# Kernel tuning notes

Measured on AMD Instinct MI355X. Metric: run time of the kernel, lower is better.

The kernel has to match this reference:

```python
import jax, jax.numpy as jnp
import numpy as np

DIM = 192
HEADS = 6
WS = 7          # window size
SS = 3          # shift size
MLP_H = int(DIM * 4.0)
EPS_LN = 1e-5


def _static_tables():
    # Swin-v2 log-spaced continuous relative coords table: (1, 2*WS-1, 2*WS-1, 2)
    ch = np.arange(-(WS - 1), WS, dtype=np.float32)
    cw = np.arange(-(WS - 1), WS, dtype=np.float32)
    t = np.stack(np.meshgrid(ch, cw, indexing='ij'), axis=-1)[None]
    t[..., 0] /= (WS - 1)
    t[..., 1] /= (WS - 1)
    t *= 7.0
    t = np.sign(t) * np.log2(np.abs(t) + 1.0) / np.log2(7.0)
    # relative position index: (WS*WS, WS*WS)
    coords = np.stack(np.meshgrid(np.arange(WS), np.arange(WS), indexing='ij'))
    cf = coords.reshape(2, -1)
    rc = (cf[:, :, None] - cf[:, None, :]).transpose(1, 2, 0)
    rc[..., 0] += WS - 1
    rc[..., 1] += WS - 1
    rc[..., 0] *= 2 * WS - 1
    rpi = rc.sum(-1)
    return jnp.asarray(t, jnp.float32), jnp.asarray(rpi, jnp.int32)


def _attn_mask(H, W):
    # shifted-window mask: (nW, N, N) with 0 / -100
    img = np.zeros((H, W), np.float32)
    cnt = 0
    for hs in (slice(0, -WS), slice(-WS, -SS), slice(-SS, None)):
        for ws in (slice(0, -WS), slice(-WS, -SS), slice(-SS, None)):
            img[hs, ws] = cnt
            cnt += 1
    mw = img.reshape(H // WS, WS, W // WS, WS).transpose(0, 2, 1, 3).reshape(-1, WS * WS)
    am = mw[:, None, :] - mw[:, :, None]
    am = np.where(am != 0, -100.0, 0.0).astype(np.float32)
    return jnp.asarray(am)


def _ln(x, w, b):
    m = x.mean(-1, keepdims=True)
    v = ((x - m) ** 2).mean(-1, keepdims=True)
    return (x - m) / jnp.sqrt(v + EPS_LN) * w + b


def setup_inputs() -> dict:
    key = jax.random.key(0)
    ks = jax.random.split(key, 16)
    d = DIM
    inp = {
        'x': jax.random.normal(ks[0], (32, 56, 56, d), jnp.float32),
        'qkv_w': jax.random.normal(ks[1], (3 * d, d), jnp.float32) * (2.0 / d) ** 0.5,
        'qkv_b': jnp.full((3 * d,), 0.01, jnp.float32),
        'proj_w': jax.random.normal(ks[2], (d, d), jnp.float32) * (2.0 / d) ** 0.5,
        'proj_b': jnp.full((d,), 0.01, jnp.float32),
        'logit_scale': jnp.log(10.0 * jnp.ones((HEADS, 1, 1), jnp.float32)),
        'cpb_w1': jax.random.normal(ks[3], (512, 2), jnp.float32) * (2.0 / 2) ** 0.5,
        'cpb_b1': jnp.full((512,), 0.01, jnp.float32),
        'cpb_w2': jax.random.normal(ks[4], (HEADS, 512), jnp.float32) * (2.0 / 512) ** 0.5,
        'norm1_w': jnp.ones((d,), jnp.float32),
        'norm1_b': jnp.zeros((d,), jnp.float32),
        'norm2_w': jnp.ones((d,), jnp.float32),
        'norm2_b': jnp.zeros((d,), jnp.float32),
        'fc1_w': jax.random.normal(ks[5], (MLP_H, d), jnp.float32) * (2.0 / d) ** 0.5,
        'fc1_b': jnp.full((MLP_H,), 0.01, jnp.float32),
        'fc2_w': jax.random.normal(ks[6], (d, MLP_H), jnp.float32) * (2.0 / MLP_H) ** 0.5,
        'fc2_b': jnp.full((d,), 0.01, jnp.float32),
    }
    return inp


def reference(x, qkv_w, qkv_b, proj_w, proj_b, logit_scale, cpb_w1, cpb_b1, cpb_w2,
              norm1_w, norm1_b, norm2_w, norm2_b, fc1_w, fc1_b, fc2_w, fc2_b):
    B, H, W, C = x.shape
    N = WS * WS
    hd = C // HEADS
    table, rpi = _static_tables()
    mask = _attn_mask(H, W)  # (nW, N, N)
    nW = mask.shape[0]

    shortcut = x
    # cyclic shift + window partition: (B*nW, N, C)
    xs = jnp.roll(x, (-SS, -SS), axis=(1, 2))
    xw = xs.reshape(B, H // WS, WS, W // WS, WS, C).transpose(0, 1, 3, 2, 4, 5).reshape(-1, N, C)

    qkv = xw @ qkv_w.T + qkv_b
    qkv = qkv.reshape(-1, N, 3, HEADS, hd).transpose(2, 0, 3, 1, 4)
    q, k, v = qkv[0], qkv[1], qkv[2]  # (B_, H, N, hd)

    qn = q / jnp.clip(jnp.linalg.norm(q, axis=-1, keepdims=True), 1e-12)
    kn = k / jnp.clip(jnp.linalg.norm(k, axis=-1, keepdims=True), 1e-12)
    scale = jnp.exp(jnp.minimum(logit_scale, jnp.log(100.0)))  # (HEADS,1,1)
    attn = jnp.einsum('bhnd,bhmd->bhnm', qn, kn) * scale

    # CPB-MLP relative position bias
    hbt = jax.nn.leaky_relu(table @ cpb_w1.T + cpb_b1, 0.01) @ cpb_w2.T  # (1,13,13,HEADS)
    bias_table = hbt.reshape(-1, HEADS)
    rpb = bias_table[rpi.reshape(-1)].reshape(N, N, HEADS).transpose(2, 0, 1)
    attn = attn + (14.0 * jax.nn.sigmoid(rpb))[None]

    # shifted-window mask + softmax
    attn = attn.reshape(B, nW, HEADS, N, N) + mask[None, :, None]
    attn = jax.nn.softmax(attn.reshape(-1, HEADS, N, N), axis=-1)

    out = jnp.einsum('bhnm,bhmd->bnhd', attn, v).reshape(-1, N, C)
    out = out @ proj_w.T + proj_b

    # window reverse + reverse shift
    out = out.reshape(B, H // WS, W // WS, WS, WS, C).transpose(0, 1, 3, 2, 4, 5).reshape(B, H, W, C)
    out = jnp.roll(out, (SS, SS), axis=(1, 2))

    # post-norm residuals (Swin-v2 style)
    x1 = shortcut + _ln(out, norm1_w, norm1_b)
    mlp = jax.nn.gelu(x1 @ fc1_w.T + fc1_b, approximate=False) @ fc2_w.T + fc2_b
    return x1 + _ln(mlp, norm2_w, norm2_b)
```

## Files before the change

### kernel.cpp

```cpp
#include <hip/hip_runtime.h>
#include <math.h>

#define CDIM 192
#define NHEADS 6
#define HDIM 32
#define WSZ 7
#define NTOK 49
#define SHIFT 3
#define HW 56
#define MLPH 768
#define NTOKENS 100352
#define QKS 576
#define XS 200
#define VTS 72
#define PPS 72
#define LS 196
#define QPS 72
#define AS2 200
#define HS2 200
#define OS2 196

typedef __attribute__((ext_vector_type(8))) short short8;
typedef __attribute__((ext_vector_type(4))) float floatx4;
typedef unsigned short ushort_t;
typedef unsigned int uint_t;

__device__ __forceinline__ ushort_t f2b(float f) {
  uint_t u = __float_as_uint(f);
  u = (u + 0x7FFFu + ((u >> 16) & 1u)) >> 16;
  return (ushort_t)u;
}

__global__ void prep_kernel(const float* __restrict__ fc1_w, const float* __restrict__ fc2_w,
                            const float* __restrict__ qkv_w, const float* __restrict__ proj_w,
                            ushort_t* __restrict__ w1b, ushort_t* __restrict__ w2b,
                            ushort_t* __restrict__ qwb, ushort_t* __restrict__ pwb) {
  int i = blockIdx.x * 256 + threadIdx.x;
  if (i < MLPH*CDIM) w1b[i] = f2b(fc1_w[i]);
  else if (i < 2*MLPH*CDIM) w2b[i - MLPH*CDIM] = f2b(fc2_w[i - MLPH*CDIM]);
  else if (i < 2*MLPH*CDIM + 3*CDIM*CDIM) qwb[i - 2*MLPH*CDIM] = f2b(qkv_w[i - 2*MLPH*CDIM]);
  else if (i < 2*MLPH*CDIM + 4*CDIM*CDIM)
    pwb[i - 2*MLPH*CDIM - 3*CDIM*CDIM] = f2b(proj_w[i - 2*MLPH*CDIM - 3*CDIM*CDIM]);
}

__global__ __launch_bounds__(256) void cpb1_kernel(const float* __restrict__ w1,
                                                   const float* __restrict__ b1,
                                                   const float* __restrict__ w2,
                                                   float* __restrict__ bt) {
  int wave = threadIdx.x >> 6, lane = threadIdx.x & 63;
  int e = blockIdx.x * 4 + wave;
  if (e >= 169) return;
  const float inv_log2_7 = 0.35620718710802217f;
  int a = e / 13, b = e % 13;
  float v0 = (float)(a - 6) * (7.0f / 6.0f);
  float v1 = (float)(b - 6) * (7.0f / 6.0f);
  float s0 = (v0 > 0.f) ? 1.f : ((v0 < 0.f) ? -1.f : 0.f);
  float s1 = (v1 > 0.f) ? 1.f : ((v1 < 0.f) ? -1.f : 0.f);
  v0 = s0 * log2f(fabsf(v0) + 1.0f) * inv_log2_7;
  v1 = s1 * log2f(fabsf(v1) + 1.0f) * inv_log2_7;
  float acc[NHEADS];
  #pragma unroll
  for (int h = 0; h < NHEADS; ++h) acc[h] = 0.f;
  #pragma unroll
  for (int j = 0; j < 8; ++j) {
    int k = lane + 64*j;
    float hv = v0 * w1[2*k] + v1 * w1[2*k+1] + b1[k];
    hv = (hv > 0.f) ? hv : 0.01f * hv;
    #pragma unroll
    for (int h = 0; h < NHEADS; ++h) acc[h] += hv * w2[h*512 + k];
  }
  #pragma unroll
  for (int m = 1; m < 64; m <<= 1)
    #pragma unroll
    for (int h = 0; h < NHEADS; ++h) acc[h] += __shfl_xor(acc[h], m, 64);
  if (lane == 0) {
    #pragma unroll
    for (int h = 0; h < NHEADS; ++h) bt[e*NHEADS + h] = acc[h];
  }
}

__global__ void cpb2_kernel(const float* __restrict__ bt, float* __restrict__ abias) {
  int e = blockIdx.x * 256 + threadIdx.x;
  if (e >= NHEADS*NTOK*NTOK) return;
  int h = e / (NTOK*NTOK);
  int r = e % (NTOK*NTOK);
  int i = r / NTOK, j = r % NTOK;
  int idx = (i/7 - j/7 + 6) * 13 + (i%7 - j%7 + 6);
  float v = bt[idx*NHEADS + h];
  abias[e] = 14.0f / (1.0f + __expf(-v));
}

__global__ __launch_bounds__(384) void qkv_kernel(
    const float* __restrict__ x, const ushort_t* __restrict__ qwb,
    const float* __restrict__ qkv_b, ushort_t* __restrict__ qkvg) {
  __shared__ __align__(16) ushort_t s_a[64*AS2];
  int tid = threadIdx.x;
  int lane = tid & 63;
  int h = tid >> 6;
  int l15 = lane & 15, quad = lane >> 4;
  size_t tbase = (size_t)blockIdx.x * 64;

  for (int e = tid; e < 64*48; e += 384) {
    int t = e / 48, cc = (e % 48) * 4;
    float4 v = *(const float4*)(x + (tbase + t)*CDIM + cc);
    uint_t p0 = (uint_t)f2b(v.x) | ((uint_t)f2b(v.y) << 16);
    uint_t p1 = (uint_t)f2b(v.z) | ((uint_t)f2b(v.w) << 16);
    *(uint_t*)&s_a[t*AS2 + cc]     = p0;
    *(uint_t*)&s_a[t*AS2 + cc + 2] = p1;
  }
  __syncthreads();

  floatx4 acc[6][4];
  #pragma unroll
  for (int nt = 0; nt < 6; ++nt)
    #pragma unroll
    for (int mt = 0; mt < 4; ++mt) acc[nt][mt] = (floatx4){0.f,0.f,0.f,0.f};
  #pragma unroll
  for (int kt = 0; kt < 6; ++kt) {
    short8 a[4];
    #pragma unroll
    for (int mt = 0; mt < 4; ++mt)
      a[mt] = *(const short8*)&s_a[(mt*16 + l15)*AS2 + kt*32 + quad*8];
    #pragma unroll
    for (int nt = 0; nt < 6; ++nt) {
      int o = (nt >> 1)*CDIM + h*HDIM + (nt & 1)*16 + l15;
      short8 b = *(const short8*)&qwb[(size_t)o*CDIM + kt*32 + quad*8];
      #pragma unroll
      for (int mt = 0; mt < 4; ++mt)
        acc[nt][mt] = __builtin_amdgcn_mfma_f32_16x16x32_bf16(a[mt], b, acc[nt][mt], 0, 0, 0);
    }
  }
  #pragma unroll
  for (int w2 = 0; w2 < 2; ++w2) {
    float b0 = qkv_b[w2*CDIM + h*HDIM + l15];
    float b1 = qkv_b[w2*CDIM + h*HDIM + 16 + l15];
    #pragma unroll
    for (int mt = 0; mt < 4; ++mt) {
      float vv[2][4], ss[4];
      #pragma unroll
      for (int r = 0; r < 4; ++r) {
        float t0 = acc[w2*2][mt][r] + b0;
        float t1 = acc[w2*2+1][mt][r] + b1;
        vv[0][r] = t0; vv[1][r] = t1;
        ss[r] = t0*t0 + t1*t1;
      }
      #pragma unroll
      for (int m = 1; m < 16; m <<= 1)
        #pragma unroll
        for (int r = 0; r < 4; ++r) ss[r] += __shfl_xor(ss[r], m, 64);
      #pragma unroll
      for (int r = 0; r < 4; ++r) {
        float inv = 1.0f / fmaxf(sqrtf(ss[r]), 1e-12f);
        size_t tok = tbase + mt*16 + quad*4 + r;
        qkvg[tok*QKS + w2*CDIM + h*HDIM + l15]      = f2b(vv[0][r] * inv);
        qkvg[tok*QKS + w2*CDIM + h*HDIM + 16 + l15] = f2b(vv[1][r] * inv);
      }
    }
  }
  {
    float b0 = qkv_b[2*CDIM + h*HDIM + l15];
    float b1 = qkv_b[2*CDIM + h*HDIM + 16 + l15];
    #pragma unroll
    for (int mt = 0; mt < 4; ++mt)
      #pragma unroll
      for (int r = 0; r < 4; ++r) {
        size_t tok = tbase + mt*16 + quad*4 + r;
        qkvg[tok*QKS + 2*CDIM + h*HDIM + l15]      = f2b(acc[4][mt][r] + b0);
        qkvg[tok*QKS + 2*CDIM + h*HDIM + 16 + l15] = f2b(acc[5][mt][r] + b1);
      }
  }
}

__global__ __launch_bounds__(512, 4) void attn_kernel(
    const float* __restrict__ x, const ushort_t* __restrict__ qkvg,
    const ushort_t* __restrict__ pwb, const float* __restrict__ proj_b,
    const float* __restrict__ logit_scale, const float* __restrict__ abias,
    const float* __restrict__ n1w, const float* __restrict__ n1b,
    float* __restrict__ outp) {
  __shared__ __align__(16) ushort_t sm[192*VTS + 128*PPS + 64*XS];
  ushort_t* s_vt = sm;
  ushort_t* s_P  = sm + 192*VTS;
  ushort_t* s_o  = s_P + 128*PPS;
  float*    s_ln = (float*)sm;
  __shared__ float s_mu[NTOK], s_rs[NTOK];
  __shared__ int s_id[64];

  int tid = threadIdx.x;
  int lane = tid & 63;
  int wave = tid >> 6;
  int wm = wave & 3, wh = wave >> 2;
  int l15 = lane & 15, quad = lane >> 4;
  int mrow0 = wm*16 + quad*4;
  int blk = blockIdx.x;
  int bimg = blk >> 6, wh_b = (blk >> 3) & 7, ww_b = blk & 7;
  int rbase = wh_b*WSZ, cbase = ww_b*WSZ;

  int ti_a = wm*16 + l15; ti_a = (ti_a < NTOK) ? ti_a : (NTOK-1);
  int ra = rbase + ti_a/7 + SHIFT; ra -= (ra >= HW) ? HW : 0;
  int ca = cbase + ti_a%7 + SHIFT; ca -= (ca >= HW) ? HW : 0;
  uint_t qrow = (uint_t)((bimg*HW + ra)*HW + ca) * QKS;
  uint_t krow[4];
  #pragma unroll
  for (int nt = 0; nt < 4; ++nt) {
    int tn = nt*16 + l15; tn = (tn < NTOK) ? tn : (NTOK-1);
    int r = rbase + tn/7 + SHIFT; r -= (r >= HW) ? HW : 0;
    int c = cbase + tn%7 + SHIFT; c -= (c >= HW) ? HW : 0;
    krow[nt] = (uint_t)((bimg*HW + r)*HW + c) * QKS + CDIM;
  }
  short8 aq[3];
  #pragma unroll
  for (int hh = 0; hh < 3; ++hh)
    aq[hh] = *(const short8*)&qkvg[(size_t)qrow + (wh*3+hh)*HDIM + quad*8];

  if (tid < NTOK) {
    int r = rbase + tid/7;
    int c = cbase + tid%7;
    int hid = (r < HW-WSZ) ? 0 : ((r < HW-SHIFT) ? 1 : 2);
    int wid = (c < HW-WSZ) ? 0 : ((c < HW-SHIFT) ? 1 : 2);
    s_id[tid] = hid*3 + wid;
  }

  for (int e = tid; e < 32*48; e += 512) {
    int tp = e & 31, dg = e >> 5;
    int t0 = 2*tp, t1 = t0 + 1;
    uint2 va = make_uint2(0u, 0u), vb = make_uint2(0u, 0u);
    if (t0 < NTOK) {
      int r = rbase + t0/7 + SHIFT; r -= (r >= HW) ? HW : 0;
      int c = cbase + t0%7 + SHIFT; c -= (c >= HW) ? HW : 0;
      va = *(const uint2*)&qkvg[((size_t)((bimg*HW + r)*HW + c))*QKS + 2*CDIM + dg*4];
    }
    if (t1 < NTOK) {
      int r = rbase + t1/7 + SHIFT; r -= (r >= HW) ? HW : 0;
      int c = cbase + t1%7 + SHIFT; c -= (c >= HW) ? HW : 0;
      vb = *(const uint2*)&qkvg[((size_t)((bimg*HW + r)*HW + c))*QKS + 2*CDIM + dg*4];
    }
    int d = dg*4;
    *(uint_t*)&s_vt[(d  )*VTS + t0] = (va.x & 0xFFFFu) | (vb.x << 16);
    *(uint_t*)&s_vt[(d+1)*VTS + t0] = (va.x >> 16) | (vb.x & 0xFFFF0000u);
    *(uint_t*)&s_vt[(d+2)*VTS + t0] = (va.y & 0xFFFFu) | (vb.y << 16);
    *(uint_t*)&s_vt[(d+3)*VTS + t0] = (va.y >> 16) | (vb.y & 0xFFFF0000u);
  }
  __syncthreads();

  ushort_t* sPh = s_P + wave*16*PPS;
  for (int hh = 0; hh < 3; ++hh) {
    int h = wh*3 + hh;
    short8 bk[4];
    #pragma unroll
    for (int nt = 0; nt < 4; ++nt)
      bk[nt] = *(const short8*)&qkvg[(size_t)krow[nt] + h*HDIM + quad*8];
    floatx4 sv[4];
    #pragma unroll
    for (int nt = 0; nt < 4; ++nt)
      sv[nt] = __builtin_amdgcn_mfma_f32_16x16x32_bf16(aq[hh], bk[nt], (floatx4){0.f,0.f,0.f,0.f}, 0, 0, 0);
    float sc = __expf(fminf(logit_scale[h], 4.6051702f));
    #pragma unroll
    for (int r = 0; r < 4; ++r) {
      int m_tok = mrow0 + r;
      int mi = (m_tok < NTOK) ? m_tok : (NTOK-1);
      float srow[4];
      float mx = -1e30f;
      #pragma unroll
      for (int nt = 0; nt < 4; ++nt) {
        int n = nt*16 + l15;
        int ni = (n < NTOK) ? n : (NTOK-1);
        float s = sv[nt][r]*sc + abias[(h*NTOK + mi)*NTOK + ni];
        if (s_id[mi] != s_id[ni]) s -= 100.f;
        if (n >= NTOK) s = -1e30f;
        srow[nt] = s;
        mx = fmaxf(mx, s);
      }
      #pragma unroll
      for (int m = 1; m < 16; m <<= 1) mx = fmaxf(mx, __shfl_xor(mx, m, 64));
      float p[4], sum = 0.f;
      #pragma unroll
      for (int nt = 0; nt < 4; ++nt) { p[nt] = __expf(srow[nt] - mx); sum += p[nt]; }
      #pragma unroll
      for (int m = 1; m < 16; m <<= 1) sum += __shfl_xor(sum, m, 64);
      float inv = 1.0f / sum;
      #pragma unroll
      for (int nt = 0; nt < 4; ++nt) {
        int n = nt*16 + l15;
        sPh[(quad*4 + r)*PPS + n] = (n < NTOK) ? f2b(p[nt]*inv) : (ushort_t)0;
      }
    }
    floatx4 ov[2];
    ov[0] = (floatx4){0.f,0.f,0.f,0.f}; ov[1] = (floatx4){0.f,0.f,0.f,0.f};
    #pragma unroll
    for (int kt = 0; kt < 2; ++kt) {
      short8 ap = *(const short8*)&sPh[l15*PPS + kt*32 + quad*8];
      #pragma unroll
      for (int dt = 0; dt < 2; ++dt) {
        short8 bv = *(const short8*)&s_vt[(h*HDIM + dt*16 + l15)*VTS + kt*32 + quad*8];
        ov[dt] = __builtin_amdgcn_mfma_f32_16x16x32_bf16(ap, bv, ov[dt], 0, 0, 0);
      }
    }
    #pragma unroll
    for (int dt = 0; dt < 2; ++dt)
      #pragma unroll
      for (int r = 0; r < 4; ++r)
        s_o[(mrow0 + r)*XS + h*HDIM + dt*16 + l15] = f2b(ov[dt][r]);
  }
  __syncthreads();

  short8 aof[6];
  #pragma unroll
  for (int kt = 0; kt < 6; ++kt)
    aof[kt] = *(const short8*)&s_o[(wm*16 + l15)*XS + kt*32 + quad*8];
  floatx4 pacc[6];
  #pragma unroll
  for (int j = 0; j < 6; ++j) pacc[j] = (floatx4){0.f,0.f,0.f,0.f};
  #pragma unroll
  for (int kt = 0; kt < 6; ++kt) {
    #pragma unroll
    for (int j = 0; j < 6; ++j) {
      int n = wh*96 + j*16 + l15;
      short8 b = *(const short8*)&pwb[(size_t)n*CDIM + kt*32 + quad*8];
      pacc[j] = __builtin_amdgcn_mfma_f32_16x16x32_bf16(aof[kt], b, pacc[j], 0, 0, 0);
    }
  }
  #pragma unroll
  for (int j = 0; j < 6; ++j) {
    int c = wh*96 + j*16 + l15;
    float pb = proj_b[c];
    #pragma unroll
    for (int r = 0; r < 4; ++r) {
      int m = mrow0 + r;
      if (m < NTOK) s_ln[m*LS + c] = pacc[j][r] + pb;
    }
  }
  __syncthreads();
  if (tid < NTOK) {
    const float4* row = (const float4*)(s_ln + tid*LS);
    float mu = 0.f;
    #pragma unroll 8
    for (int c = 0; c < 48; ++c) { float4 v = row[c]; mu += v.x+v.y+v.z+v.w; }
    mu *= (1.0f/CDIM);
    float var = 0.f;
    #pragma unroll 8
    for (int c = 0; c < 48; ++c) {
      float4 v = row[c];
      float a0=v.x-mu, a1=v.y-mu, a2=v.z-mu, a3=v.w-mu;
      var += a0*a0 + a1*a1 + a2*a2 + a3*a3;
    }
    var *= (1.0f/CDIM);
    s_mu[tid] = mu; s_rs[tid] = rsqrtf(var + 1e-5f);
  }
  __syncthreads();
  for (int e = tid; e < NTOK*48; e += 512) {
    int ti = e / 48, cc = (e % 48) * 4;
    int r = (rbase + ti/WSZ + SHIFT) % HW;
    int cl = (cbase + ti%WSZ + SHIFT) % HW;
    size_t g = (((size_t)bimg*HW + r)*HW + cl)*CDIM + cc;
    float4 xv = *(const float4*)(x + g);
    float4 wv = *(const float4*)(n1w + cc);
    float4 bv = *(const float4*)(n1b + cc);
    float mu = s_mu[ti], rs = s_rs[ti];
    float4 o;
    o.x = xv.x + (s_ln[ti*LS+cc  ] - mu)*rs*wv.x + bv.x;
    o.y = xv.y + (s_ln[ti*LS+cc+1] - mu)*rs*wv.y + bv.y;
    o.z = xv.z + (s_ln[ti*LS+cc+2] - mu)*rs*wv.z + bv.z;
    o.w = xv.w + (s_ln[ti*LS+cc+3] - mu)*rs*wv.w + bv.w;
    *(float4*)(outp + g) = o;
  }
}

__global__ __launch_bounds__(512, 4) void attn_fused(
    const float* __restrict__ x, const ushort_t* __restrict__ qwb,
    const float* __restrict__ qkv_b, const ushort_t* __restrict__ pwb,
    const float* __restrict__ proj_b, const float* __restrict__ logit_scale,
    const float* __restrict__ abias, const float* __restrict__ n1w,
    const float* __restrict__ n1b, float* __restrict__ outp) {
  __shared__ __align__(16) ushort_t sm[64*XS + 2*64*QPS + 64*VTS + 2*64*PPS];
  ushort_t* s_x  = sm;
  ushort_t* s_qn = s_x  + 64*XS;
  ushort_t* s_kn = s_qn + 64*QPS;
  ushort_t* s_vt = s_kn + 64*QPS;
  ushort_t* s_P  = s_vt + 64*VTS;
  ushort_t* s_o  = s_x;
  float*    s_ln = (float*)sm;
  __shared__ float s_mu[NTOK], s_rs[NTOK];
  __shared__ int s_id[NTOK];

  int tid = threadIdx.x;
  int lane = tid & 63;
  int wave = tid >> 6;
  int wm = wave & 3, wh = wave >> 2;
  int l15 = lane & 15, quad = lane >> 4;
  int mrow0 = wm*16 + quad*4;
  int blk = blockIdx.x;
  int bimg = blk >> 6, wh_b = (blk >> 3) & 7, ww_b = blk & 7;

  for (int e = tid; e < 64*48; e += 512) {
    int i = e / 48, cc = (e % 48) * 4;
    uint_t p0 = 0, p1 = 0;
    if (i < NTOK) {
      int r = (wh_b*WSZ + i/WSZ + SHIFT) % HW;
      int c = (ww_b*WSZ + i%WSZ + SHIFT) % HW;
      float4 v = *(const float4*)(x + (((size_t)bimg*HW + r)*HW + c)*CDIM + cc);
      p0 = (uint_t)f2b(v.x) | ((uint_t)f2b(v.y) << 16);
      p1 = (uint_t)f2b(v.z) | ((uint_t)f2b(v.w) << 16);
    }
    *(uint_t*)&s_x[i*XS + cc]     = p0;
    *(uint_t*)&s_x[i*XS + cc + 2] = p1;
  }
  if (tid < NTOK) {
    int r = wh_b*WSZ + tid/WSZ;
    int c = ww_b*WSZ + tid%WSZ;
    int hid = (r < HW-WSZ) ? 0 : ((r < HW-SHIFT) ? 1 : 2);
    int wid = (c < HW-WSZ) ? 0 : ((c < HW-SHIFT) ? 1 : 2);
    s_id[tid] = hid*3 + wid;
  }
  __syncthreads();

  short8 axf[6];
  #pragma unroll
  for (int kt = 0; kt < 6; ++kt)
    axf[kt] = *(const short8*)&s_x[(wm*16 + l15)*XS + kt*32 + quad*8];

  for (int g = 0; g < 3; ++g) {
    int h = g*2 + wh;
    floatx4 acc[6];
    #pragma unroll
    for (int nt = 0; nt < 6; ++nt) acc[nt] = (floatx4){0.f,0.f,0.f,0.f};
    #pragma unroll
    for (int kt = 0; kt < 6; ++kt) {
      short8 a = axf[kt];
      #pragma unroll
      for (int nt = 0; nt < 6; ++nt) {
        int o = (nt >> 1)*CDIM + h*HDIM + (nt & 1)*16 + l15;
        short8 b = *(const short8*)&qwb[(size_t)o*CDIM + kt*32 + quad*8];
        acc[nt] = __builtin_amdgcn_mfma_f32_16x16x32_bf16(a, b, acc[nt], 0, 0, 0);
      }
    }
    #pragma unroll
    for (int w2 = 0; w2 < 2; ++w2) {
      float vv[2][4], ss[4];
      #pragma unroll
      for (int r = 0; r < 4; ++r) ss[r] = 0.f;
      #pragma unroll
      for (int dt = 0; dt < 2; ++dt) {
        float bias = qkv_b[w2*CDIM + h*HDIM + dt*16 + l15];
        #pragma unroll
        for (int r = 0; r < 4; ++r) {
          float t = acc[w2*2 + dt][r] + bias;
          vv[dt][r] = t; ss[r] += t*t;
        }
      }
      #pragma unroll
      for (int m = 1; m < 16; m <<= 1)
        #pragma unroll
        for (int r = 0; r < 4; ++r) ss[r] += __shfl_xor(ss[r], m, 64);
      ushort_t* dst = w2 ? s_kn : s_qn;
      #pragma unroll
      for (int r = 0; r < 4; ++r) {
        float inv = 1.0f / fmaxf(sqrtf(ss[r]), 1e-12f);
        #pragma unroll
        for (int dt = 0; dt < 2; ++dt)
          dst[(mrow0 + r)*QPS + wh*HDIM + dt*16 + l15] = f2b(vv[dt][r] * inv);
      }
    }
    #pragma unroll
    for (int dt = 0; dt < 2; ++dt) {
      float bias = qkv_b[2*CDIM + h*HDIM + dt*16 + l15];
      int d = wh*HDIM + dt*16 + l15;
      #pragma unroll
      for (int rp = 0; rp < 2; ++rp) {
        uint_t pk = (uint_t)f2b(acc[4+dt][2*rp] + bias) |
                    ((uint_t)f2b(acc[4+dt][2*rp+1] + bias) << 16);
        *(uint_t*)&s_vt[d*VTS + mrow0 + 2*rp] = pk;
      }
    }
    __syncthreads();

    short8 aq = *(const short8*)&s_qn[(wm*16 + l15)*QPS + wh*HDIM + quad*8];
    floatx4 sv[4];
    #pragma unroll
    for (int nt = 0; nt < 4; ++nt) {
      short8 bk = *(const short8*)&s_kn[(nt*16 + l15)*QPS + wh*HDIM + quad*8];
      sv[nt] = __builtin_amdgcn_mfma_f32_16x16x32_bf16(aq, bk, (floatx4){0.f,0.f,0.f,0.f}, 0, 0, 0);
    }
    float sc = __expf(fminf(logit_scale[h], 4.6051702f));
    ushort_t* sPh = s_P + wh*64*PPS;
    #pragma unroll
    for (int r = 0; r < 4; ++r) {
      int m_tok = mrow0 + r;
      int mi = (m_tok < NTOK) ? m_tok : (NTOK-1);
      float srow[4];
      float mx = -1e30f;
      #pragma unroll
      for (int nt = 0; nt < 4; ++nt) {
        int n = nt*16 + l15;
        int ni = (n < NTOK) ? n : (NTOK-1);
        float s = sv[nt][r]*sc + abias[(h*NTOK + mi)*NTOK + ni];
        if (s_id[mi] != s_id[ni]) s -= 100.f;
        if (n >= NTOK) s = -1e30f;
        srow[nt] = s;
        mx = fmaxf(mx, s);
      }
      #pragma unroll
      for (int m = 1; m < 16; m <<= 1) mx = fmaxf(mx, __shfl_xor(mx, m, 64));
      float p[4], sum = 0.f;
      #pragma unroll
      for (int nt = 0; nt < 4; ++nt) { p[nt] = __expf(srow[nt] - mx); sum += p[nt]; }
      #pragma unroll
      for (int m = 1; m < 16; m <<= 1) sum += __shfl_xor(sum, m, 64);
      float inv = 1.0f / sum;
      #pragma unroll
      for (int nt = 0; nt < 4; ++nt) {
        int n = nt*16 + l15;
        sPh[(mrow0 + r)*PPS + n] = (n < NTOK) ? f2b(p[nt]*inv) : (ushort_t)0;
      }
    }
    floatx4 ov[2];
    ov[0] = (floatx4){0.f,0.f,0.f,0.f}; ov[1] = (floatx4){0.f,0.f,0.f,0.f};
    #pragma unroll
    for (int kt = 0; kt < 2; ++kt) {
      short8 ap = *(const short8*)&sPh[(wm*16 + l15)*PPS + kt*32 + quad*8];
      #pragma unroll
      for (int dt = 0; dt < 2; ++dt) {
        short8 bv = *(const short8*)&s_vt[(wh*HDIM + dt*16 + l15)*VTS + kt*32 + quad*8];
        ov[dt] = __builtin_amdgcn_mfma_f32_16x16x32_bf16(ap, bv, ov[dt], 0, 0, 0);
      }
    }
    #pragma unroll
    for (int dt = 0; dt < 2; ++dt)
      #pragma unroll
      for (int r = 0; r < 4; ++r)
        s_o[(mrow0 + r)*XS + h*HDIM + dt*16 + l15] = f2b(ov[dt][r]);
    __syncthreads();
  }

  short8 aof[6];
  #pragma unroll
  for (int kt = 0; kt < 6; ++kt)
    aof[kt] = *(const short8*)&s_o[(wm*16 + l15)*XS + kt*32 + quad*8];
  __syncthreads();
  floatx4 pacc[6];
  #pragma unroll
  for (int j = 0; j < 6; ++j) pacc[j] = (floatx4){0.f,0.f,0.f,0.f};
  #pragma unroll
  for (int kt = 0; kt < 6; ++kt) {
    #pragma unroll
    for (int j = 0; j < 6; ++j) {
      int n = wh*96 + j*16 + l15;
      short8 b = *(const short8*)&pwb[(size_t)n*CDIM + kt*32 + quad*8];
      pacc[j] = __builtin_amdgcn_mfma_f32_16x16x32_bf16(aof[kt], b, pacc[j], 0, 0, 0);
    }
  }
  #pragma unroll
  for (int j = 0; j < 6; ++j) {
    int c = wh*96 + j*16 + l15;
    float pb = proj_b[c];
    #pragma unroll
    for (int r = 0; r < 4; ++r) {
      int m = mrow0 + r;
      if (m < NTOK) s_ln[m*LS + c] = pacc[j][r] + pb;
    }
  }
  __syncthreads();
  if (tid < NTOK) {
    const float4* row = (const float4*)(s_ln + tid*LS);
    float mu = 0.f;
    #pragma unroll 8
    for (int c = 0; c < 48; ++c) { float4 v = row[c]; mu += v.x+v.y+v.z+v.w; }
    mu *= (1.0f/CDIM);
    float var = 0.f;
    #pragma unroll 8
    for (int c = 0; c < 48; ++c) {
      float4 v = row[c];
      float a0=v.x-mu, a1=v.y-mu, a2=v.z-mu, a3=v.w-mu;
      var += a0*a0 + a1*a1 + a2*a2 + a3*a3;
    }
    var *= (1.0f/CDIM);
    s_mu[tid] = mu; s_rs[tid] = rsqrtf(var + 1e-5f);
  }
  __syncthreads();
  for (int e = tid; e < NTOK*48; e += 512) {
    int ti = e / 48, cc = (e % 48) * 4;
    int r = (wh_b*WSZ + ti/WSZ + SHIFT) % HW;
    int cl = (ww_b*WSZ + ti%WSZ + SHIFT) % HW;
    size_t g = (((size_t)bimg*HW + r)*HW + cl)*CDIM + cc;
    float4 xv = *(const float4*)(x + g);
    float4 wv = *(const float4*)(n1w + cc);
    float4 bv = *(const float4*)(n1b + cc);
    float mu = s_mu[ti], rs = s_rs[ti];
    float4 o;
    o.x = xv.x + (s_ln[ti*LS+cc  ] - mu)*rs*wv.x + bv.x;
    o.y = xv.y + (s_ln[ti*LS+cc+1] - mu)*rs*wv.y + bv.y;
    o.z = xv.z + (s_ln[ti*LS+cc+2] - mu)*rs*wv.z + bv.z;
    o.w = xv.w + (s_ln[ti*LS+cc+3] - mu)*rs*wv.w + bv.w;
    *(float4*)(outp + g) = o;
  }
}

__global__ __launch_bounds__(256) void mlp_kernel(
    const ushort_t* __restrict__ w1b, const ushort_t* __restrict__ w2b,
    const float* __restrict__ fc1_b, const float* __restrict__ fc2_b,
    const float* __restrict__ n2w, const float* __restrict__ n2b,
    float* __restrict__ io) {
  __shared__ __align__(16) ushort_t sm2[64*AS2 + 64*HS2];
  ushort_t* s_a = sm2;
  ushort_t* s_h = sm2 + 64*AS2;
  float*    s_o = (float*)sm2;
  __shared__ float s_mu[64], s_rs[64];

  int tid = threadIdx.x;
  int lane = tid & 63;
  int wave = tid >> 6;
  int l15 = lane & 15, quad = lane >> 4;
  size_t base = (size_t)blockIdx.x * (64*CDIM);

  for (int e = tid; e < 64*48; e += 256) {
    int t = e / 48, cc = (e % 48) * 4;
    float4 v = *(const float4*)(io + base + t*CDIM + cc);
    uint_t p0 = (uint_t)f2b(v.x) | ((uint_t)f2b(v.y) << 16);
    uint_t p1 = (uint_t)f2b(v.z) | ((uint_t)f2b(v.w) << 16);
    *(uint_t*)&s_a[t*AS2 + cc]     = p0;
    *(uint_t*)&s_a[t*AS2 + cc + 2] = p1;
  }
  __syncthreads();

  floatx4 oacc[12];
  #pragma unroll
  for (int t = 0; t < 12; ++t) oacc[t] = (floatx4){0.f,0.f,0.f,0.f};

  for (int ch = 0; ch < 4; ++ch) {
    floatx4 hacc[12];
    #pragma unroll
    for (int t = 0; t < 12; ++t) hacc[t] = (floatx4){0.f,0.f,0.f,0.f};
    #pragma unroll
    for (int kt = 0; kt < 6; ++kt) {
      short8 a[4];
      #pragma unroll
      for (int mt = 0; mt < 4; ++mt)
        a[mt] = *(const short8*)&s_a[(mt*16 + l15)*AS2 + kt*32 + quad*8];
      #pragma unroll
      for (int nt = 0; nt < 3; ++nt) {
        int n = ch*192 + wave*48 + nt*16 + l15;
        short8 b = *(const short8*)&w1b[(size_t)n*CDIM + kt*32 + quad*8];
        #pragma unroll
        for (int mt = 0; mt < 4; ++mt)
          hacc[nt*4+mt] = __builtin_amdgcn_mfma_f32_16x16x32_bf16(a[mt], b, hacc[nt*4+mt], 0, 0, 0);
      }
    }
    #pragma unroll
    for (int nt = 0; nt < 3; ++nt) {
      int n = ch*192 + wave*48 + nt*16 + l15;
      int cloc = wave*48 + nt*16 + l15;
      float bias = fc1_b[n];
      #pragma unroll
      for (int mt = 0; mt < 4; ++mt) {
        #pragma unroll
        for (int r = 0; r < 4; ++r) {
          float v = hacc[nt*4+mt][r] + bias;
          v = 0.5f * v * (1.0f + erff(v * 0.70710678118654752f));
          s_h[(mt*16 + quad*4 + r)*HS2 + cloc] = f2b(v);
        }
      }
    }
    __syncthreads();
    #pragma unroll
    for (int kt = 0; kt < 6; ++kt) {
      short8 a2[4];
      #pragma unroll
      for (int mt = 0; mt < 4; ++mt)
        a2[mt] = *(const short8*)&s_h[(mt*16 + l15)*HS2 + kt*32 + quad*8];
      #pragma unroll
      for (int nt = 0; nt < 3; ++nt) {
        int n2 = wave*48 + nt*16 + l15;
        short8 b2 = *(const short8*)&w2b[(size_t)n2*MLPH + ch*192 + kt*32 + quad*8];
        #pragma unroll
        for (int mt = 0; mt < 4; ++mt)
          oacc[nt*4+mt] = __builtin_amdgcn_mfma_f32_16x16x32_bf16(a2[mt], b2, oacc[nt*4+mt], 0, 0, 0);
      }
    }
    __syncthreads();
  }

  #pragma unroll
  for (int nt = 0; nt < 3; ++nt) {
    int c = wave*48 + nt*16 + l15;
    float bb = fc2_b[c];
    #pragma unroll
    for (int mt = 0; mt < 4; ++mt) {
      #pragma unroll
      for (int r = 0; r < 4; ++r)
        s_o[(mt*16 + quad*4 + r)*OS2 + c] = oacc[nt*4+mt][r] + bb;
    }
  }
  __syncthreads();
  if (tid < 64) {
    const float4* row = (const float4*)(s_o + tid*OS2);
    float mu = 0.f;
    #pragma unroll 8
    for (int c = 0; c < 48; ++c) { float4 v = row[c]; mu += v.x+v.y+v.z+v.w; }
    mu *= (1.0f/CDIM);
    float var = 0.f;
    #pragma unroll 8
    for (int c = 0; c < 48; ++c) {
      float4 v = row[c];
      float a0=v.x-mu, a1=v.y-mu, a2=v.z-mu, a3=v.w-mu;
      var += a0*a0 + a1*a1 + a2*a2 + a3*a3;
    }
    var *= (1.0f/CDIM);
    s_mu[tid] = mu; s_rs[tid] = rsqrtf(var + 1e-5f);
  }
  __syncthreads();
  for (int e = tid; e < 64*48; e += 256) {
    int t = e / 48, cc = (e % 48) * 4;
    float4 xv = *(const float4*)(io + base + t*CDIM + cc);
    float4 wv = *(const float4*)(n2w + cc);
    float4 bv = *(const float4*)(n2b + cc);
    float mu = s_mu[t], rs = s_rs[t];
    float4 o;
    o.x = xv.x + (s_o[t*OS2+cc  ] - mu)*rs*wv.x + bv.x;
    o.y = xv.y + (s_o[t*OS2+cc+1] - mu)*rs*wv.y + bv.y;
    o.z = xv.z + (s_o[t*OS2+cc+2] - mu)*rs*wv.z + bv.z;
    o.w = xv.w + (s_o[t*OS2+cc+3] - mu)*rs*wv.w + bv.w;
    *(float4*)(io + base + t*CDIM + cc) = o;
  }
}

extern "C" void kernel_launch(void* const* d_in, const int* in_sizes, int n_in,
                              void* d_out, int out_size, void* d_ws, size_t ws_size,
                              hipStream_t stream) {
  const float* x           = (const float*)d_in[0];
  const float* qkv_w       = (const float*)d_in[1];
  const float* qkv_b       = (const float*)d_in[2];
  const float* proj_w      = (const float*)d_in[3];
  const float* proj_b      = (const float*)d_in[4];
  const float* logit_scale = (const float*)d_in[5];
  const float* cpb_w1      = (const float*)d_in[6];
  const float* cpb_b1      = (const float*)d_in[7];
  const float* cpb_w2      = (const float*)d_in[8];
  const float* n1w         = (const float*)d_in[9];
  const float* n1b         = (const float*)d_in[10];
  const float* n2w         = (const float*)d_in[11];
  const float* n2b         = (const float*)d_in[12];
  const float* fc1_w       = (const float*)d_in[13];
  const float* fc1_b       = (const float*)d_in[14];
  const float* fc2_w       = (const float*)d_in[15];
  const float* fc2_b       = (const float*)d_in[16];
  float* out = (float*)d_out;

  ushort_t* w1b = (ushort_t*)d_ws;
  ushort_t* w2b = w1b + MLPH*CDIM;
  ushort_t* qwb = w2b + CDIM*MLPH;
  ushort_t* pwb = qwb + 3*CDIM*CDIM;
  float* abias  = (float*)(pwb + CDIM*CDIM);
  float* bt     = abias + NHEADS*NTOK*NTOK;
  ushort_t* qkvg = (ushort_t*)(bt + 169*NHEADS);

  size_t needed = (size_t)(2*MLPH*CDIM + 4*CDIM*CDIM)*2
                + (size_t)(NHEADS*NTOK*NTOK)*4 + (size_t)(169*NHEADS)*4
                + (size_t)NTOKENS*QKS*2;
  bool split = ws_size >= needed;

  int prep_elems = 2*MLPH*CDIM + 4*CDIM*CDIM;
  hipLaunchKernelGGL(prep_kernel, dim3((prep_elems + 255)/256), dim3(256), 0, stream,
                     fc1_w, fc2_w, qkv_w, proj_w, w1b, w2b, qwb, pwb);
  hipLaunchKernelGGL(cpb1_kernel, dim3((169 + 3)/4), dim3(256), 0, stream,
                     cpb_w1, cpb_b1, cpb_w2, bt);
  hipLaunchKernelGGL(cpb2_kernel, dim3((NHEADS*NTOK*NTOK + 255)/256), dim3(256), 0, stream,
                     bt, abias);
  if (split) {
    hipLaunchKernelGGL(qkv_kernel, dim3(NTOKENS/64), dim3(384), 0, stream,
                       x, qwb, qkv_b, qkvg);
    hipLaunchKernelGGL(attn_kernel, dim3(2048), dim3(512), 0, stream,
                       x, qkvg, pwb, proj_b, logit_scale, abias, n1w, n1b, out);
  } else {
    hipLaunchKernelGGL(attn_fused, dim3(2048), dim3(512), 0, stream,
                       x, qwb, qkv_b, pwb, proj_b, logit_scale, abias, n1w, n1b, out);
  }
  hipLaunchKernelGGL(mlp_kernel, dim3(NTOKENS/64), dim3(256), 0, stream,
                     w1b, w2b, fc1_b, fc2_b, n2w, n2b, out);
}
```

Before: 672.9 us.

## Restructure MLP kernel to 512 threads with full hidden tile in LDS and fast GELU

The MLP kernel now uses 512 threads (8 waves). It computes the whole 768-wide hidden activation for a 64-token tile in one pass and stores it in LDS, instead of looping over four hidden chunks with syncs between them. The second GEMM splits the work into 4 row groups by 2 column halves across waves. The exact erf GELU is replaced by a tanh-style sigmoid approximation using __expf, which is cheaper but deviates slightly from the reference erf GELU. LDS use grows to about 150KB per block, which limits occupancy to one block per CU.

Result: slower. 811.5 us (+20.6%).

```diff
diff --git a/kernel.cpp b/kernel.cpp
--- a/kernel.cpp
+++ b/kernel.cpp
@@ -17,8 +17,7 @@
 #define LS 196
 #define QPS 72
 #define AS2 200
-#define HS2 200
-#define OS2 196
+#define HPS 776
 
 typedef __attribute__((ext_vector_type(8))) short short8;
 typedef __attribute__((ext_vector_type(4))) float floatx4;
@@ -29,6 +28,12 @@
   uint_t u = __float_as_uint(f);
   u = (u + 0x7FFFu + ((u >> 16) & 1u)) >> 16;
   return (ushort_t)u;
+}
+
+__device__ __forceinline__ float gelu_fast(float v) {
+  float u2 = 1.5957691f * v * (1.0f + 0.044715f * v * v);
+  float s = 1.0f / (1.0f + __expf(-u2));
+  return v * s;
 }
 
 __global__ void prep_kernel(const float* __restrict__ fc1_w, const float* __restrict__ fc2_w,
@@ -594,26 +599,26 @@
   }
 }
 
-__global__ __launch_bounds__(256) void mlp_kernel(
+__global__ __launch_bounds__(512) void mlp_fused(
     const ushort_t* __restrict__ w1b, const ushort_t* __restrict__ w2b,
     const float* __restrict__ fc1_b, const float* __restrict__ fc2_b,
     const float* __restrict__ n2w, const float* __restrict__ n2b,
     float* __restrict__ io) {
-  __shared__ __align__(16) ushort_t sm2[64*AS2 + 64*HS2];
-  ushort_t* s_a = sm2;
-  ushort_t* s_h = sm2 + 64*AS2;
-  float*    s_o = (float*)sm2;
+  __shared__ __align__(16) ushort_t s_h[64*HPS];
+  __shared__ __align__(16) float s_ln[64*LS];
   __shared__ float s_mu[64], s_rs[64];
+  ushort_t* s_a = s_h;
 
   int tid = threadIdx.x;
   int lane = tid & 63;
   int wave = tid >> 6;
+  int wm = wave & 3, wh = wave >> 2;
   int l15 = lane & 15, quad = lane >> 4;
-  size_t base = (size_t)blockIdx.x * (64*CDIM);
-
-  for (int e = tid; e < 64*48; e += 256) {
+  size_t tbase = (size_t)blockIdx.x * 64;
+
+  for (int e = tid; e < 64*48; e += 512) {
     int t = e / 48, cc = (e % 48) * 4;
-    float4 v = *(const float4*)(io + base + t*CDIM + cc);
+    float4 v = *(const float4*)(io + (tbase + t)*CDIM + cc);
     uint_t p0 = (uint_t)f2b(v.x) | ((uint_t)f2b(v.y) << 16);
     uint_t p1 = (uint_t)f2b(v.z) | ((uint_t)f2b(v.w) << 16);
     *(uint_t*)&s_a[t*AS2 + cc]     = p0;
@@ -621,77 +626,67 @@
   }
   __syncthreads();
 
-  floatx4 oacc[12];
-  #pragma unroll
-  for (int t = 0; t < 12; ++t) oacc[t] = (floatx4){0.f,0.f,0.f,0.f};
-
-  for (int ch = 0; ch < 4; ++ch) {
-    floatx4 hacc[12];
-    #pragma unroll
-    for (int t = 0; t < 12; ++t) hacc[t] = (floatx4){0.f,0.f,0.f,0.f};
-    #pragma unroll
-    for (int kt = 0; kt < 6; ++kt) {
-      short8 a[4];
+  floatx4 acc1[6][4];
+  #pragma unroll
+  for (int nt = 0; nt < 6; ++nt)
+    #pragma unroll
+    for (int mt = 0; mt < 4; ++mt) acc1[nt][mt] = (floatx4){0.f,0.f,0.f,0.f};
+  #pragma unroll
+  for (int kt = 0; kt < 6; ++kt) {
+    short8 a[4];
+    #pragma unroll
+    for (int mt = 0; mt < 4; ++mt)
+      a[mt] = *(const short8*)&s_a[(mt*16 + l15)*AS2 + kt*32 + quad*8];
+    #pragma unroll
+    for (int nt = 0; nt < 6; ++nt) {
+      int n = wave*96 + nt*16 + l15;
+      short8 b = *(const short8*)&w1b[(size_t)n*CDIM + kt*32 + quad*8];
       #pragma unroll
       for (int mt = 0; mt < 4; ++mt)
-        a[mt] = *(const short8*)&s_a[(mt*16 + l15)*AS2 + kt*32 + quad*8];
-      #pragma unroll
-      for (int nt = 0; nt < 3; ++nt) {
-        int n = ch*192 + wave*48 + nt*16 + l15;
-        short8 b = *(const short8*)&w1b[(size_t)n*CDIM + kt*32 + quad*8];
-        #pragma unroll
-        for (int mt = 0; mt < 4; ++mt)
-          hacc[nt*4+mt] = __builtin_amdgcn_mfma_f32_16x16x32_bf16(a[mt], b, hacc[nt*4+mt], 0, 0, 0);
-      }
-    }
-    #pragma unroll
-    for (int nt = 0; nt < 3; ++nt) {
-      int n = ch*192 + wave*48 + nt*16 + l15;
-      int cloc = wave*48 + nt*16 + l15;
-      float bias = fc1_b[n];
-      #pragma unroll
-      for (int mt = 0; mt < 4; ++mt) {
-        #pragma unroll
-        for (int r = 0; r < 4; ++r) {
-          float v = hacc[nt*4+mt][r] + bias;
-          v = 0.5f * v * (1.0f + erff(v * 0.70710678118654752f));
-          s_h[(mt*16 + quad*4 + r)*HS2 + cloc] = f2b(v);
-        }
-      }
-    }
-    __syncthreads();
-    #pragma unroll
-    for (int kt = 0; kt < 6; ++kt) {
-      short8 a2[4];
-      #pragma unroll
-      for (int mt = 0; mt < 4; ++mt)
-        a2[mt] = *(const short8*)&s_h[(mt*16 + l15)*HS2 + kt*32 + quad*8];
-      #pragma unroll
-      for (int nt = 0; nt < 3; ++nt) {
-        int n2 = wave*48 + nt*16 + l15;
-        short8 b2 = *(const short8*)&w2b[(size_t)n2*MLPH + ch*192 + kt*32 + quad*8];
-        #pragma unroll
-        for (int mt = 0; mt < 4; ++mt)
-          oacc[nt*4+mt] = __builtin_amdgcn_mfma_f32_16x16x32_bf16(a2[mt], b2, oacc[nt*4+mt], 0, 0, 0);
-      }
-    }
-    __syncthreads();
-  }
-
-  #pragma unroll
-  for (int nt = 0; nt < 3; ++nt) {
-    int c = wave*48 + nt*16 + l15;
+        acc1[nt][mt] = __builtin_amdgcn_mfma_f32_16x16x32_bf16(a[mt], b, acc1[nt][mt], 0, 0, 0);
+    }
+  }
+  __syncthreads();
+
+  #pragma unroll
+  for (int nt = 0; nt < 6; ++nt) {
+    int n = wave*96 + nt*16 + l15;
+    float bias = fc1_b[n];
+    #pragma unroll
+    for (int mt = 0; mt < 4; ++mt) {
+      #pragma unroll
+      for (int r = 0; r < 4; ++r) {
+        float v = acc1[nt][mt][r] + bias;
+        s_h[(mt*16 + quad*4 + r)*HPS + n] = f2b(gelu_fast(v));
+      }
+    }
+  }
+  __syncthreads();
+
+  floatx4 acc2[6];
+  #pragma unroll
+  for (int nt = 0; nt < 6; ++nt) acc2[nt] = (floatx4){0.f,0.f,0.f,0.f};
+  #pragma unroll 4
+  for (int kt = 0; kt < 24; ++kt) {
+    short8 a = *(const short8*)&s_h[(wm*16 + l15)*HPS + kt*32 + quad*8];
+    #pragma unroll
+    for (int nt = 0; nt < 6; ++nt) {
+      int n = wh*96 + nt*16 + l15;
+      short8 b = *(const short8*)&w2b[(size_t)n*MLPH + kt*32 + quad*8];
+      acc2[nt] = __builtin_amdgcn_mfma_f32_16x16x32_bf16(a, b, acc2[nt], 0, 0, 0);
+    }
+  }
+  #pragma unroll
+  for (int nt = 0; nt < 6; ++nt) {
+    int c = wh*96 + nt*16 + l15;
     float bb = fc2_b[c];
     #pragma unroll
-    for (int mt = 0; mt < 4; ++mt) {
-      #pragma unroll
-      for (int r = 0; r < 4; ++r)
-        s_o[(mt*16 + quad*4 + r)*OS2 + c] = oacc[nt*4+mt][r] + bb;
-    }
+    for (int r = 0; r < 4; ++r)
+      s_ln[(wm*16 + quad*4 + r)*LS + c] = acc2[nt][r] + bb;
   }
   __syncthreads();
   if (tid < 64) {
-    const float4* row = (const float4*)(s_o + tid*OS2);
+    const float4* row = (const float4*)(s_ln + tid*LS);
     float mu = 0.f;
     #pragma unroll 8
     for (int c = 0; c < 48; ++c) { float4 v = row[c]; mu += v.x+v.y+v.z+v.w; }
@@ -707,18 +702,18 @@
     s_mu[tid] = mu; s_rs[tid] = rsqrtf(var + 1e-5f);
   }
   __syncthreads();
-  for (int e = tid; e < 64*48; e += 256) {
+  for (int e = tid; e < 64*48; e += 512) {
     int t = e / 48, cc = (e % 48) * 4;
-    float4 xv = *(const float4*)(io + base + t*CDIM + cc);
+    float4 xv = *(const float4*)(io + (tbase + t)*CDIM + cc);
     float4 wv = *(const float4*)(n2w + cc);
     float4 bv = *(const float4*)(n2b + cc);
     float mu = s_mu[t], rs = s_rs[t];
     float4 o;
-    o.x = xv.x + (s_o[t*OS2+cc  ] - mu)*rs*wv.x + bv.x;
-    o.y = xv.y + (s_o[t*OS2+cc+1] - mu)*rs*wv.y + bv.y;
-    o.z = xv.z + (s_o[t*OS2+cc+2] - mu)*rs*wv.z + bv.z;
-    o.w = xv.w + (s_o[t*OS2+cc+3] - mu)*rs*wv.w + bv.w;
-    *(float4*)(io + base + t*CDIM + cc) = o;
+    o.x = xv.x + (s_ln[t*LS+cc  ] - mu)*rs*wv.x + bv.x;
+    o.y = xv.y + (s_ln[t*LS+cc+1] - mu)*rs*wv.y + bv.y;
+    o.z = xv.z + (s_ln[t*LS+cc+2] - mu)*rs*wv.z + bv.z;
+    o.w = xv.w + (s_ln[t*LS+cc+3] - mu)*rs*wv.w + bv.w;
+    *(float4*)(io + (tbase + t)*CDIM + cc) = o;
   }
 }
 
@@ -752,10 +747,10 @@
   float* bt     = abias + NHEADS*NTOK*NTOK;
   ushort_t* qkvg = (ushort_t*)(bt + 169*NHEADS);
 
-  size_t needed = (size_t)(2*MLPH*CDIM + 4*CDIM*CDIM)*2
-                + (size_t)(NHEADS*NTOK*NTOK)*4 + (size_t)(169*NHEADS)*4
-                + (size_t)NTOKENS*QKS*2;
-  bool split = ws_size >= needed;
+  size_t base_b = (size_t)(2*MLPH*CDIM + 4*CDIM*CDIM)*2
+                + (size_t)(NHEADS*NTOK*NTOK)*4 + (size_t)(169*NHEADS)*4;
+  size_t qkvg_b = (size_t)NTOKENS*QKS*2;
+  bool split_qkv = ws_size >= base_b + qkvg_b;
 
   int prep_elems = 2*MLPH*CDIM + 4*CDIM*CDIM;
   hipLaunchKernelGGL(prep_kernel, dim3((prep_elems + 255)/256), dim3(256), 0, stream,
@@ -764,7 +759,7 @@
                      cpb_w1, cpb_b1, cpb_w2, bt);
   hipLaunchKernelGGL(cpb2_kernel, dim3((NHEADS*NTOK*NTOK + 255)/256), dim3(256), 0, stream,
                      bt, abias);
-  if (split) {
+  if (split_qkv) {
     hipLaunchKernelGGL(qkv_kernel, dim3(NTOKENS/64), dim3(384), 0, stream,
                        x, qwb, qkv_b, qkvg);
     hipLaunchKernelGGL(attn_kernel, dim3(2048), dim3(512), 0, stream,
@@ -773,6 +768,6 @@
     hipLaunchKernelGGL(attn_fused, dim3(2048), dim3(512), 0, stream,
                        x, qwb, qkv_b, pwb, proj_b, logit_scale, abias, n1w, n1b, out);
   }
-  hipLaunchKernelGGL(mlp_kernel, dim3(NTOKENS/64), dim3(256), 0, stream,
+  hipLaunchKernelGGL(mlp_fused, dim3(NTOKENS/64), dim3(512), 0, stream,
                      w1b, w2b, fc1_b, fc2_b, n2w, n2b, out);
 }
```
